# Performance work log

Hardware: AMD Instinct MI355X
Metric: run time of the kernel (lower is better)

## Reference

```python
import jax, jax.numpy as jnp
import numpy as np

B, S, D, H = 2, 2048, 1024, 16
DK = D // H


def setup_inputs() -> dict:
    key = jax.random.key(0)
    ks = jax.random.split(key, 12)
    s = 1.0 / np.sqrt(D)
    inp = {
        "key": jax.random.normal(ks[0], (B, S, D), jnp.float32),
        "query": jax.random.normal(ks[1], (B, S, D), jnp.float32),
        "value": jax.random.normal(ks[2], (B, S, D), jnp.float32),
        # causal mask, broadcastable to (B, H, S, S)
        "mask": jnp.tril(jnp.ones((S, S), jnp.int32))[None, None, :, :],
        "Wq": jax.random.normal(ks[3], (D, D), jnp.float32) * s,
        "bq": jax.random.normal(ks[4], (D,), jnp.float32) * s,
        "Wk": jax.random.normal(ks[5], (D, D), jnp.float32) * s,
        "bk": jax.random.normal(ks[6], (D,), jnp.float32) * s,
        "Wv": jax.random.normal(ks[7], (D, D), jnp.float32) * s,
        "bv": jax.random.normal(ks[8], (D,), jnp.float32) * s,
        "Wo": jax.random.normal(ks[9], (D, D), jnp.float32) * s,
        "bo": jax.random.normal(ks[10], (D,), jnp.float32) * s,
    }
    return inp


def reference(key, query, value, mask, Wq, bq, Wk, bk, Wv, bv, Wo, bo):
    # Linear projections (torch nn.Linear: x @ W.T + b)
    k = key @ Wk.T + bk
    q = query @ Wq.T + bq
    v = value @ Wv.T + bv
    # Faithful to source: raw view (B, H, S, DK), NO transpose --
    # this splits the SEQUENCE dim across heads, matching the original code.
    k = k.reshape(B, H, S, DK)
    q = q.reshape(B, H, S, DK)
    v = v.reshape(B, H, S, DK)
    # Scores scaled by sqrt(d_model) (as in source, not sqrt(d_k))
    scores = jnp.einsum('bhqd,bhkd->bhqk', q, k) / jnp.sqrt(jnp.float32(D))
    scores = jnp.where(mask == 0, -jnp.inf, scores)
    attn = jax.nn.softmax(scores, axis=-1)  # dropout p=0.0 -> identity
    x = jnp.einsum('bhqk,bhkd->bhqd', attn, v)
    # Faithful raw view merge: (B, H, S, DK) -> (B, S, H*DK)
    x = x.reshape(B, S, H * DK)
    return x @ Wo.T + bo
```

## Files before the change

kernel.cpp:

```cpp
#include <hip/hip_runtime.h>
#include <stdint.h>

typedef unsigned short u16;
typedef __attribute__((ext_vector_type(8))) short bfrag8;
typedef __attribute__((ext_vector_type(4))) float f32x4;
typedef __attribute__((ext_vector_type(8))) unsigned short u16x8;
typedef __attribute__((ext_vector_type(4))) unsigned short u16x4;

__device__ __forceinline__ u16 f2bf(float f) {
  union { float f; uint32_t u; } v; v.f = f;
  return (u16)((v.u + 0x7FFFu + ((v.u >> 16) & 1u)) >> 16);
}

__device__ __forceinline__ uint32_t cvtpk_bf16(float a, float b) {
  uint32_t r;
  asm("v_cvt_pk_bf16_f32 %0, %1, %2" : "=v"(r) : "v"(a), "v"(b));
  return r;
}

__device__ __forceinline__ void gload16(const void* g, void* l) {
  __builtin_amdgcn_global_load_lds(
      (const __attribute__((address_space(1))) void*)g,
      (__attribute__((address_space(3))) void*)l, 16, 0, 0);
}

struct CvtJob { const float* src; u16* dst; int n4; };
struct CvtBatch { CvtJob j[7]; };

__global__ void cvt_batch(CvtBatch b) {
  CvtJob jb = b.j[blockIdx.y];
  int i = blockIdx.x * blockDim.x + threadIdx.x;
  if (i >= jb.n4) return;
  float4 v = reinterpret_cast<const float4*>(jb.src)[i];
  u16x4 o;
  o[0] = f2bf(v.x); o[1] = f2bf(v.y); o[2] = f2bf(v.z); o[3] = f2bf(v.w);
  reinterpret_cast<u16x4*>(jb.dst)[i] = o;
}

struct Gemm3 {
  const u16* A[3];
  const u16* W[3];
  const float* bias[3];
  void* C[3];
};

template<int OUT_F32, int BM, int BN, int MINW>
__global__ __launch_bounds__(256, MINW) void gemm_nt_bias(Gemm3 g) {
  constexpr int K = 1024, N = 1024;
  constexpr int BK = 64;
  constexpr int WM = BM / 32, WN = BN / 32;
  __shared__ __align__(16) u16 As[2][BM][BK];
  __shared__ __align__(16) u16 Bs[2][BN][BK];
  const int z = blockIdx.z;
  const u16* __restrict__ A = g.A[z];
  const u16* __restrict__ W = g.W[z];
  const float* __restrict__ bias = g.bias[z];
  const int tid = threadIdx.x, lane = tid & 63, wave = tid >> 6;
  const int lr = lane & 15, lg = lane >> 4;
  const int wr = (wave >> 1) * (WM * 16), wc = (wave & 1) * (WN * 16);
  const int bm = blockIdx.x * BM, bn = blockIdx.y * BN;
  const int srow = lane >> 3;
  const int schunk = (lane & 7) ^ srow;

  f32x4 acc[WM][WN] = {};

  auto STAGE = [&](int k0, int bufi) {
#pragma unroll
    for (int i = 0; i < BM / 32; i++) {
      int r = wave * (BM / 4) + i * 8;
      gload16(A + (size_t)(bm + r + srow) * K + k0 + schunk * 8, &As[bufi][r][0]);
    }
#pragma unroll
    for (int i = 0; i < BN / 32; i++) {
      int r = wave * (BN / 4) + i * 8;
      gload16(W + (size_t)(bn + r + srow) * K + k0 + schunk * 8, &Bs[bufi][r][0]);
    }
  };

  STAGE(0, 0);
  __syncthreads();
  int buf = 0;

  for (int k0 = 0; k0 < K; k0 += BK) {
    if (k0 + BK < K) STAGE(k0 + BK, buf ^ 1);
    bfrag8 af[2][WM], bf[2][WN];
#pragma unroll
    for (int ks = 0; ks < 2; ks++) {
#pragma unroll
      for (int mi = 0; mi < WM; mi++) {
        const int row = wr + mi * 16 + lr;
        af[ks][mi] = *(const bfrag8*)&As[buf][row][((ks * 4 + lg) ^ (row & 7)) * 8];
      }
#pragma unroll
      for (int ni = 0; ni < WN; ni++) {
        const int row = wc + ni * 16 + lr;
        bf[ks][ni] = *(const bfrag8*)&Bs[buf][row][((ks * 4 + lg) ^ (row & 7)) * 8];
      }
    }
#pragma unroll
    for (int ks = 0; ks < 2; ks++)
#pragma unroll
      for (int mi = 0; mi < WM; mi++)
#pragma unroll
        for (int ni = 0; ni < WN; ni++)
          acc[mi][ni] = __builtin_amdgcn_mfma_f32_16x16x32_bf16(af[ks][mi], bf[ks][ni], acc[mi][ni], 0, 0, 0);
    __syncthreads();
    buf ^= 1;
  }

  const int col0 = bn + wc + lr;
#pragma unroll
  for (int ni = 0; ni < WN; ni++) {
    int col = col0 + ni * 16;
    float bv = bias[col];
#pragma unroll
    for (int mi = 0; mi < WM; mi++) {
      int row = bm + wr + mi * 16 + lg * 4;
#pragma unroll
      for (int r = 0; r < 4; r++) {
        float v = acc[mi][ni][r] + bv;
        if (OUT_F32)
          ((float*)g.C[z])[(size_t)(row + r) * N + col] = v;
        else
          ((u16*)g.C[z])[(size_t)(row + r) * N + col] = f2bf(v);
      }
    }
  }
}

__global__ void vtrans_kernel(const u16* __restrict__ Vp, u16* __restrict__ VT,
                              unsigned* __restrict__ ctr) {
  if (blockIdx.x == 0 && blockIdx.y == 0 && threadIdx.x < 8) ctr[threadIdx.x * 16] = 0u;
  __shared__ u16 T[64][66];
  const int kt = blockIdx.x, bh = blockIdx.y;
  const int tid = threadIdx.x;
  const u16* src = Vp + (size_t)bh * 131072 + (size_t)kt * 64 * 64;
#pragma unroll
  for (int i = 0; i < 2; i++) {
    int u = tid + 256 * i;
    int row = u >> 3, c = (u & 7) * 8;
    u16x8 v = *(const u16x8*)(src + row * 64 + c);
#pragma unroll
    for (int j = 0; j < 8; j++) T[c + j][row] = v[j];
  }
  __syncthreads();
  u16* dst = VT + (size_t)bh * 131072 + (size_t)kt * 64;
#pragma unroll
  for (int i = 0; i < 2; i++) {
    int u = tid + 256 * i;
    int d = u >> 3, c = (u & 7) * 8;
    u16x8 o = *(const u16x8*)&T[d][c];
    *(u16x8*)(dst + (size_t)d * 2048 + c) = o;
  }
}

__global__ __launch_bounds__(256, 3) void attn_kernel(
    const u16* __restrict__ Qp, const u16* __restrict__ Kp,
    const u16* __restrict__ VT, u16* __restrict__ X,
    unsigned* __restrict__ ctr)
{
  __shared__ __align__(16) u16 Ks[2][64][64];
  __shared__ __align__(16) u16 Vs[2][64][64];
  constexpr int LDP = 72;
  __shared__ __align__(16) u16 Ps[4][16][LDP];
  __shared__ unsigned s_unit;

  const int tid = threadIdx.x, lane = tid & 63, w = tid >> 6;
  const int lr = lane & 15, lg = lane >> 4;
  const int grp = (int)(blockIdx.x & 7);
  unsigned* __restrict__ gctr = ctr + grp * 16;
  const int srow = lane >> 3;
  const int schunk = (lane & 7) ^ srow;
  const float C2 = 0.045084939f;
  const float THR = 11.5f;

  for (;;) {
    __syncthreads();
    if (tid == 0) s_unit = atomicAdd(gctr, 1u);
    __syncthreads();
    const unsigned u = s_unit;
    if (u >= 128u) return;
    const int j = 31 - (int)(u >> 2);
    const int bh = grp * 4 + (int)(u & 3u);
    const size_t base = (size_t)bh * 131072;
    const u16* __restrict__ Qb = Qp + base;
    const u16* __restrict__ Kb = Kp + base;
    const u16* __restrict__ Vtb = VT + base;
    const int qrow0 = j * 64 + w * 16;
    const int q = qrow0 + lr;

    bfrag8 qf[2];
#pragma unroll
    for (int ds = 0; ds < 2; ds++)
      qf[ds] = *(const bfrag8*)(Qb + (size_t)(qrow0 + lr) * 64 + ds * 32 + lg * 8);

    f32x4 oacc[4] = {};
    float m_run = -INFINITY, l_run = 0.f;

    auto STAGE = [&](int kt, int bufi) {
      const u16* gk = Kb + (size_t)(kt * 64 + w * 16 + srow) * 64 + schunk * 8;
      gload16(gk,       &Ks[bufi][w * 16][0]);
      gload16(gk + 512, &Ks[bufi][w * 16 + 8][0]);
      const u16* gv = Vtb + (size_t)(w * 16 + srow) * 2048 + kt * 64 + schunk * 8;
      gload16(gv,            &Vs[bufi][w * 16][0]);
      gload16(gv + 8 * 2048, &Vs[bufi][w * 16 + 8][0]);
    };

    STAGE(0, 0);
    __syncthreads();
    int buf = 0;

    for (int kt = 0; kt <= j; kt++) {
      if (kt < j) STAGE(kt + 1, buf ^ 1);

      f32x4 sacc[4];
#pragma unroll
      for (int kf = 0; kf < 4; kf++) sacc[kf] = (f32x4){0.f, 0.f, 0.f, 0.f};
#pragma unroll
      for (int kf = 0; kf < 4; kf++) {
        const int krow = kf * 16 + lr;
        bfrag8 kb0 = *(const bfrag8*)&Ks[buf][krow][((lg) ^ (krow & 7)) * 8];
        bfrag8 kb1 = *(const bfrag8*)&Ks[buf][krow][((lg + 4) ^ (krow & 7)) * 8];
        sacc[kf] = __builtin_amdgcn_mfma_f32_16x16x32_bf16(kb0, qf[0], sacc[kf], 0, 0, 0);
        sacc[kf] = __builtin_amdgcn_mfma_f32_16x16x32_bf16(kb1, qf[1], sacc[kf], 0, 0, 0);
      }

      if (kt == j) {
#pragma unroll
        for (int kf = 0; kf < 4; kf++)
#pragma unroll
          for (int r = 0; r < 4; r++) {
            int kg = kt * 64 + kf * 16 + lg * 4 + r;
            if (kg > q) sacc[kf][r] = -INFINITY;
          }
      }

      float a0 = fmaxf(fmaxf(sacc[0][0], sacc[0][1]), fmaxf(sacc[0][2], sacc[0][3]));
      float a1 = fmaxf(fmaxf(sacc[1][0], sacc[1][1]), fmaxf(sacc[1][2], sacc[1][3]));
      float a2 = fmaxf(fmaxf(sacc[2][0], sacc[2][1]), fmaxf(sacc[2][2], sacc[2][3]));
      float a3 = fmaxf(fmaxf(sacc[3][0], sacc[3][1]), fmaxf(sacc[3][2], sacc[3][3]));
      float smax = fmaxf(fmaxf(a0, a1), fmaxf(a2, a3));
      smax = fmaxf(smax, __shfl_xor(smax, 16));
      smax = fmaxf(smax, __shfl_xor(smax, 32));
      float pmax = smax * C2;
      float mnew = m_run;
      if (!__all(pmax <= m_run + THR)) {
        mnew = fmaxf(m_run, pmax);
        float corr = __builtin_amdgcn_exp2f(m_run - mnew);
        l_run *= corr;
#pragma unroll
        for (int df = 0; df < 4; df++)
#pragma unroll
          for (int r = 0; r < 4; r++) oacc[df][r] *= corr;
        m_run = mnew;
      }

      float rs = 0.f;
#pragma unroll
      for (int kf = 0; kf < 4; kf++) {
        float p0 = __builtin_amdgcn_exp2f(__builtin_fmaf(sacc[kf][0], C2, -mnew));
        float p1 = __builtin_amdgcn_exp2f(__builtin_fmaf(sacc[kf][1], C2, -mnew));
        float p2 = __builtin_amdgcn_exp2f(__builtin_fmaf(sacc[kf][2], C2, -mnew));
        float p3 = __builtin_amdgcn_exp2f(__builtin_fmaf(sacc[kf][3], C2, -mnew));
        rs += (p0 + p1) + (p2 + p3);
        uint2 pk;
        pk.x = cvtpk_bf16(p0, p1);
        pk.y = cvtpk_bf16(p2, p3);
        *(uint2*)&Ps[w][lr][kf * 16 + lg * 4] = pk;
      }
      rs += __shfl_xor(rs, 16);
      rs += __shfl_xor(rs, 32);
      l_run += rs;

#pragma unroll
      for (int ks = 0; ks < 2; ks++) {
        bfrag8 pa = *(const bfrag8*)&Ps[w][lr][ks * 32 + lg * 8];
#pragma unroll
        for (int df = 0; df < 4; df++) {
          const int vrow = df * 16 + lr;
          bfrag8 vf = *(const bfrag8*)&Vs[buf][vrow][((ks * 4 + lg) ^ (vrow & 7)) * 8];
          oacc[df] = __builtin_amdgcn_mfma_f32_16x16x32_bf16(vf, pa, oacc[df], 0, 0, 0);
        }
      }

      __syncthreads();
      buf ^= 1;
    }

    float inv = 1.0f / l_run;
#pragma unroll
    for (int df = 0; df < 4; df++) {
      u16x4 o;
#pragma unroll
      for (int r = 0; r < 4; r++) o[r] = f2bf(oacc[df][r] * inv);
      *(u16x4*)&X[base + (size_t)q * 64 + df * 16 + lg * 4] = o;
    }
  }
}

extern "C" void kernel_launch(void* const* d_in, const int* in_sizes, int n_in,
                              void* d_out, int out_size, void* d_ws, size_t ws_size,
                              hipStream_t stream) {
  const float* key   = (const float*)d_in[0];
  const float* query = (const float*)d_in[1];
  const float* value = (const float*)d_in[2];
  const float* Wq = (const float*)d_in[4];
  const float* bq = (const float*)d_in[5];
  const float* Wk = (const float*)d_in[6];
  const float* bk = (const float*)d_in[7];
  const float* Wv = (const float*)d_in[8];
  const float* bv = (const float*)d_in[9];
  const float* Wo = (const float*)d_in[10];
  const float* bo = (const float*)d_in[11];

  u16* ws = (u16*)d_ws;
  const size_t MD = 4096ull * 1024ull;
  u16* qb  = ws;
  u16* kb  = ws + MD;
  u16* vbf = ws + 2 * MD;
  u16* Qp  = ws + 3 * MD;
  u16* Kp  = ws + 4 * MD;
  u16* Vp  = ws + 5 * MD;
  u16* Xb  = ws + 6 * MD;
  u16* wqb = ws + 7 * MD;
  u16* wkb = wqb + 1024 * 1024;
  u16* wvb = wkb + 1024 * 1024;
  u16* wob = wvb + 1024 * 1024;

  CvtBatch cb;
  cb.j[0] = { query, qb, 1048576 };
  cb.j[1] = { key,   kb, 1048576 };
  cb.j[2] = { value, vbf, 1048576 };
  cb.j[3] = { Wq, wqb, 262144 };
  cb.j[4] = { Wk, wkb, 262144 };
  cb.j[5] = { Wv, wvb, 262144 };
  cb.j[6] = { Wo, wob, 262144 };
  cvt_batch<<<dim3(4096, 7), 256, 0, stream>>>(cb);

  Gemm3 g1;
  g1.A[0] = qb;  g1.A[1] = kb;  g1.A[2] = vbf;
  g1.W[0] = wqb; g1.W[1] = wkb; g1.W[2] = wvb;
  g1.bias[0] = bq; g1.bias[1] = bk; g1.bias[2] = bv;
  g1.C[0] = Qp; g1.C[1] = Kp; g1.C[2] = Vp;
  gemm_nt_bias<0, 128, 64, 3><<<dim3(32, 16, 3), 256, 0, stream>>>(g1);

  u16* VT = vbf;
  unsigned* ctr = (unsigned*)qb;
  vtrans_kernel<<<dim3(32, 32), 256, 0, stream>>>(Vp, VT, ctr);

  attn_kernel<<<768, 256, 0, stream>>>(Qp, Kp, VT, Xb, ctr);

  Gemm3 g2;
  g2.A[0] = Xb; g2.W[0] = wob; g2.bias[0] = bo; g2.C[0] = d_out;
  g2.A[1] = g2.A[2] = nullptr; g2.W[1] = g2.W[2] = nullptr;
  g2.bias[1] = g2.bias[2] = nullptr; g2.C[1] = g2.C[2] = nullptr;
  gemm_nt_bias<1, 128, 64, 3><<<dim3(32, 16, 1), 256, 0, stream>>>(g2);
}
```

Before: 123.5 us.

## Fuse fp32-to-bf16 conversion into GEMM tile loads, drop separate convert kernel

Removes the standalone conversion kernel that turned the fp32 activations and weights into bf16 buffers. The GEMM kernel now reads fp32 tiles into registers, converts them with packed cvt instructions and writes them into swizzled LDS, prefetching one tile ahead. This saves a kernel launch and a round trip of bf16 data through global memory. In exchange the GEMM reads twice as many bytes per tile, re-converts each weight tile for every block that uses it, and holds more registers for the prefetch buffers, which may lower occupancy.

```diff
diff --git a/kernel.cpp b/kernel.cpp
--- a/kernel.cpp
+++ b/kernel.cpp
@@ -24,27 +24,14 @@
       (__attribute__((address_space(3))) void*)l, 16, 0, 0);
 }
 
-struct CvtJob { const float* src; u16* dst; int n4; };
-struct CvtBatch { CvtJob j[7]; };
-
-__global__ void cvt_batch(CvtBatch b) {
-  CvtJob jb = b.j[blockIdx.y];
-  int i = blockIdx.x * blockDim.x + threadIdx.x;
-  if (i >= jb.n4) return;
-  float4 v = reinterpret_cast<const float4*>(jb.src)[i];
-  u16x4 o;
-  o[0] = f2bf(v.x); o[1] = f2bf(v.y); o[2] = f2bf(v.z); o[3] = f2bf(v.w);
-  reinterpret_cast<u16x4*>(jb.dst)[i] = o;
-}
-
 struct Gemm3 {
-  const u16* A[3];
-  const u16* W[3];
+  const void* A[3];
+  const void* W[3];
   const float* bias[3];
   void* C[3];
 };
 
-template<int OUT_F32, int BM, int BN, int MINW>
+template<int OUT_F32, int AF32, int WF32, int BM, int BN, int MINW>
 __global__ __launch_bounds__(256, MINW) void gemm_nt_bias(Gemm3 g) {
   constexpr int K = 1024, N = 1024;
   constexpr int BK = 64;
@@ -52,8 +39,8 @@
   __shared__ __align__(16) u16 As[2][BM][BK];
   __shared__ __align__(16) u16 Bs[2][BN][BK];
   const int z = blockIdx.z;
-  const u16* __restrict__ A = g.A[z];
-  const u16* __restrict__ W = g.W[z];
+  const void* __restrict__ Ap = g.A[z];
+  const void* __restrict__ Wp = g.W[z];
   const float* __restrict__ bias = g.bias[z];
   const int tid = threadIdx.x, lane = tid & 63, wave = tid >> 6;
   const int lr = lane & 15, lg = lane >> 4;
@@ -61,28 +48,92 @@
   const int bm = blockIdx.x * BM, bn = blockIdx.y * BN;
   const int srow = lane >> 3;
   const int schunk = (lane & 7) ^ srow;
+  const int frow = lane >> 4;
+  const int fcol = (lane & 15) * 4;
+  const int fchunk = (lane & 15) >> 1;
+  const int fhalf = (lane & 1) * 4;
 
   f32x4 acc[WM][WN] = {};
-
-  auto STAGE = [&](int k0, int bufi) {
-#pragma unroll
-    for (int i = 0; i < BM / 32; i++) {
-      int r = wave * (BM / 4) + i * 8;
-      gload16(A + (size_t)(bm + r + srow) * K + k0 + schunk * 8, &As[bufi][r][0]);
-    }
-#pragma unroll
-    for (int i = 0; i < BN / 32; i++) {
-      int r = wave * (BN / 4) + i * 8;
-      gload16(W + (size_t)(bn + r + srow) * K + k0 + schunk * 8, &Bs[bufi][r][0]);
-    }
-  };
-
-  STAGE(0, 0);
+  float4 ra[AF32 ? BM / 16 : 1];
+  float4 rw[WF32 ? BN / 16 : 1];
+
+  auto LOAD_A = [&](int k0) {
+    if constexpr (AF32) {
+      const float* Af = (const float*)Ap;
+#pragma unroll
+      for (int i = 0; i < BM / 16; i++) {
+        int row = wave * (BM / 4) + i * 4 + frow;
+        ra[i] = *(const float4*)(Af + (size_t)(bm + row) * K + k0 + fcol);
+      }
+    }
+  };
+  auto WRITE_A = [&](int bufi) {
+    if constexpr (AF32) {
+#pragma unroll
+      for (int i = 0; i < BM / 16; i++) {
+        int row = wave * (BM / 4) + i * 4 + frow;
+        uint2 p;
+        p.x = cvtpk_bf16(ra[i].x, ra[i].y);
+        p.y = cvtpk_bf16(ra[i].z, ra[i].w);
+        *(uint2*)&As[bufi][row][(fchunk ^ (row & 7)) * 8 + fhalf] = p;
+      }
+    }
+  };
+  auto GLOAD_A = [&](int k0, int bufi) {
+    if constexpr (!AF32) {
+      const u16* Ab = (const u16*)Ap;
+#pragma unroll
+      for (int i = 0; i < BM / 32; i++) {
+        int r = wave * (BM / 4) + i * 8;
+        gload16(Ab + (size_t)(bm + r + srow) * K + k0 + schunk * 8, &As[bufi][r][0]);
+      }
+    }
+  };
+  auto LOAD_W = [&](int k0) {
+    if constexpr (WF32) {
+      const float* Wf = (const float*)Wp;
+#pragma unroll
+      for (int i = 0; i < BN / 16; i++) {
+        int row = wave * (BN / 4) + i * 4 + frow;
+        rw[i] = *(const float4*)(Wf + (size_t)(bn + row) * K + k0 + fcol);
+      }
+    }
+  };
+  auto WRITE_W = [&](int bufi) {
+    if constexpr (WF32) {
+#pragma unroll
+      for (int i = 0; i < BN / 16; i++) {
+        int row = wave * (BN / 4) + i * 4 + frow;
+        uint2 p;
+        p.x = cvtpk_bf16(rw[i].x, rw[i].y);
+        p.y = cvtpk_bf16(rw[i].z, rw[i].w);
+        *(uint2*)&Bs[bufi][row][(fchunk ^ (row & 7)) * 8 + fhalf] = p;
+      }
+    }
+  };
+  auto GLOAD_W = [&](int k0, int bufi) {
+    if constexpr (!WF32) {
+      const u16* Wb = (const u16*)Wp;
+#pragma unroll
+      for (int i = 0; i < BN / 32; i++) {
+        int r = wave * (BN / 4) + i * 8;
+        gload16(Wb + (size_t)(bn + r + srow) * K + k0 + schunk * 8, &Bs[bufi][r][0]);
+      }
+    }
+  };
+
+  LOAD_A(0); LOAD_W(0);
+  WRITE_A(0); WRITE_W(0);
+  GLOAD_A(0, 0); GLOAD_W(0, 0);
   __syncthreads();
   int buf = 0;
 
   for (int k0 = 0; k0 < K; k0 += BK) {
-    if (k0 + BK < K) STAGE(k0 + BK, buf ^ 1);
+    const bool pf = (k0 + BK < K);
+    if (pf) {
+      GLOAD_A(k0 + BK, buf ^ 1); GLOAD_W(k0 + BK, buf ^ 1);
+      LOAD_A(k0 + BK); LOAD_W(k0 + BK);
+    }
     bfrag8 af[2][WM], bf[2][WN];
 #pragma unroll
     for (int ks = 0; ks < 2; ks++) {
@@ -104,6 +155,7 @@
 #pragma unroll
         for (int ni = 0; ni < WN; ni++)
           acc[mi][ni] = __builtin_amdgcn_mfma_f32_16x16x32_bf16(af[ks][mi], bf[ks][ni], acc[mi][ni], 0, 0, 0);
+    if (pf) { WRITE_A(buf ^ 1); WRITE_W(buf ^ 1); }
     __syncthreads();
     buf ^= 1;
   }
@@ -315,44 +367,29 @@
 
   u16* ws = (u16*)d_ws;
   const size_t MD = 4096ull * 1024ull;
-  u16* qb  = ws;
-  u16* kb  = ws + MD;
-  u16* vbf = ws + 2 * MD;
+  u16* scratch = ws;
+  u16* vtbuf = ws + 2 * MD;
   u16* Qp  = ws + 3 * MD;
   u16* Kp  = ws + 4 * MD;
   u16* Vp  = ws + 5 * MD;
   u16* Xb  = ws + 6 * MD;
-  u16* wqb = ws + 7 * MD;
-  u16* wkb = wqb + 1024 * 1024;
-  u16* wvb = wkb + 1024 * 1024;
-  u16* wob = wvb + 1024 * 1024;
-
-  CvtBatch cb;
-  cb.j[0] = { query, qb, 1048576 };
-  cb.j[1] = { key,   kb, 1048576 };
-  cb.j[2] = { value, vbf, 1048576 };
-  cb.j[3] = { Wq, wqb, 262144 };
-  cb.j[4] = { Wk, wkb, 262144 };
-  cb.j[5] = { Wv, wvb, 262144 };
-  cb.j[6] = { Wo, wob, 262144 };
-  cvt_batch<<<dim3(4096, 7), 256, 0, stream>>>(cb);
 
   Gemm3 g1;
-  g1.A[0] = qb;  g1.A[1] = kb;  g1.A[2] = vbf;
-  g1.W[0] = wqb; g1.W[1] = wkb; g1.W[2] = wvb;
+  g1.A[0] = query; g1.A[1] = key; g1.A[2] = value;
+  g1.W[0] = Wq;    g1.W[1] = Wk;  g1.W[2] = Wv;
   g1.bias[0] = bq; g1.bias[1] = bk; g1.bias[2] = bv;
   g1.C[0] = Qp; g1.C[1] = Kp; g1.C[2] = Vp;
-  gemm_nt_bias<0, 128, 64, 3><<<dim3(32, 16, 3), 256, 0, stream>>>(g1);
-
-  u16* VT = vbf;
-  unsigned* ctr = (unsigned*)qb;
+  gemm_nt_bias<0, 1, 1, 128, 64, 3><<<dim3(32, 16, 3), 256, 0, stream>>>(g1);
+
+  u16* VT = vtbuf;
+  unsigned* ctr = (unsigned*)scratch;
   vtrans_kernel<<<dim3(32, 32), 256, 0, stream>>>(Vp, VT, ctr);
 
   attn_kernel<<<768, 256, 0, stream>>>(Qp, Kp, VT, Xb, ctr);
 
   Gemm3 g2;
-  g2.A[0] = Xb; g2.W[0] = wob; g2.bias[0] = bo; g2.C[0] = d_out;
+  g2.A[0] = Xb; g2.W[0] = Wo; g2.bias[0] = bo; g2.C[0] = d_out;
   g2.A[1] = g2.A[2] = nullptr; g2.W[1] = g2.W[2] = nullptr;
   g2.bias[1] = g2.bias[2] = nullptr; g2.C[1] = g2.C[2] = nullptr;
-  gemm_nt_bias<1, 128, 64, 3><<<dim3(32, 16, 1), 256, 0, stream>>>(g2);
-}
+  gemm_nt_bias<1, 0, 1, 128, 64, 3><<<dim3(32, 16, 1), 256, 0, stream>>>(g2);
+}
```

Result: slower. 128.2 us (+3.8%).

## Double attention key tile to 128 and interleave softmax with PV per half

Applied to the files above, without the earlier changes.

The attention inner loop now processes 128 keys per iteration instead of 64. K and V^T staging is widened to match, with a 16-chunk XOR swizzle for V. The exp/pack of P and the PV MFMAs are split into two 64-key halves so the small per-wave P buffer can be reused. This halves the number of block barriers and online-softmax rescale checks per query tile. In exchange it uses more LDS and registers: occupancy drops from 3 to 2 blocks per CU, the grid shrinks to 512, and the masked diagonal tile can waste up to 64 extra keys of compute.

```diff
diff --git a/kernel.cpp b/kernel.cpp
--- a/kernel.cpp
+++ b/kernel.cpp
@@ -154,13 +154,13 @@
   }
 }
 
-__global__ __launch_bounds__(256, 3) void attn_kernel(
+__global__ __launch_bounds__(256, 2) void attn_kernel(
     const u16* __restrict__ Qp, const u16* __restrict__ Kp,
     const u16* __restrict__ VT, u16* __restrict__ X,
     unsigned* __restrict__ ctr)
 {
-  __shared__ __align__(16) u16 Ks[2][64][64];
-  __shared__ __align__(16) u16 Vs[2][64][64];
+  __shared__ __align__(16) u16 Ks[2][128][64];
+  __shared__ __align__(16) u16 Vs[2][64][128];
   constexpr int LDP = 72;
   __shared__ __align__(16) u16 Ps[4][16][LDP];
   __shared__ unsigned s_unit;
@@ -169,8 +169,10 @@
   const int lr = lane & 15, lg = lane >> 4;
   const int grp = (int)(blockIdx.x & 7);
   unsigned* __restrict__ gctr = ctr + grp * 16;
-  const int srow = lane >> 3;
-  const int schunk = (lane & 7) ^ srow;
+  const int srow8 = lane >> 3;
+  const int schunk8 = (lane & 7) ^ srow8;
+  const int srow4 = lane >> 4;
+  const int lane16 = lane & 15;
   const float C2 = 0.045084939f;
   const float THR = 11.5f;
 
@@ -198,26 +200,34 @@
     float m_run = -INFINITY, l_run = 0.f;
 
     auto STAGE = [&](int kt, int bufi) {
-      const u16* gk = Kb + (size_t)(kt * 64 + w * 16 + srow) * 64 + schunk * 8;
-      gload16(gk,       &Ks[bufi][w * 16][0]);
-      gload16(gk + 512, &Ks[bufi][w * 16 + 8][0]);
-      const u16* gv = Vtb + (size_t)(w * 16 + srow) * 2048 + kt * 64 + schunk * 8;
-      gload16(gv,            &Vs[bufi][w * 16][0]);
-      gload16(gv + 8 * 2048, &Vs[bufi][w * 16 + 8][0]);
+#pragma unroll
+      for (int i = 0; i < 4; i++) {
+        int r = w * 32 + i * 8;
+        gload16(Kb + (size_t)(kt * 128 + r + srow8) * 64 + schunk8 * 8, &Ks[bufi][r][0]);
+      }
+#pragma unroll
+      for (int i = 0; i < 4; i++) {
+        int r = w * 16 + i * 4;
+        int row = r + srow4;
+        gload16(Vtb + (size_t)row * 2048 + kt * 128 + (lane16 ^ (row & 15)) * 8,
+                &Vs[bufi][r][0]);
+      }
     };
+
+    const int ktmax = (j * 64 + 63) >> 7;
 
     STAGE(0, 0);
     __syncthreads();
     int buf = 0;
 
-    for (int kt = 0; kt <= j; kt++) {
-      if (kt < j) STAGE(kt + 1, buf ^ 1);
-
-      f32x4 sacc[4];
-#pragma unroll
-      for (int kf = 0; kf < 4; kf++) sacc[kf] = (f32x4){0.f, 0.f, 0.f, 0.f};
-#pragma unroll
-      for (int kf = 0; kf < 4; kf++) {
+    for (int kt = 0; kt <= ktmax; kt++) {
+      if (kt < ktmax) STAGE(kt + 1, buf ^ 1);
+
+      f32x4 sacc[8];
+#pragma unroll
+      for (int kf = 0; kf < 8; kf++) sacc[kf] = (f32x4){0.f, 0.f, 0.f, 0.f};
+#pragma unroll
+      for (int kf = 0; kf < 8; kf++) {
         const int krow = kf * 16 + lr;
         bfrag8 kb0 = *(const bfrag8*)&Ks[buf][krow][((lg) ^ (krow & 7)) * 8];
         bfrag8 kb1 = *(const bfrag8*)&Ks[buf][krow][((lg + 4) ^ (krow & 7)) * 8];
@@ -225,21 +235,26 @@
         sacc[kf] = __builtin_amdgcn_mfma_f32_16x16x32_bf16(kb1, qf[1], sacc[kf], 0, 0, 0);
       }
 
-      if (kt == j) {
-#pragma unroll
-        for (int kf = 0; kf < 4; kf++)
+      if (kt == ktmax) {
+#pragma unroll
+        for (int kf = 0; kf < 8; kf++)
 #pragma unroll
           for (int r = 0; r < 4; r++) {
-            int kg = kt * 64 + kf * 16 + lg * 4 + r;
+            int kg = kt * 128 + kf * 16 + lg * 4 + r;
             if (kg > q) sacc[kf][r] = -INFINITY;
           }
       }
 
-      float a0 = fmaxf(fmaxf(sacc[0][0], sacc[0][1]), fmaxf(sacc[0][2], sacc[0][3]));
-      float a1 = fmaxf(fmaxf(sacc[1][0], sacc[1][1]), fmaxf(sacc[1][2], sacc[1][3]));
-      float a2 = fmaxf(fmaxf(sacc[2][0], sacc[2][1]), fmaxf(sacc[2][2], sacc[2][3]));
-      float a3 = fmaxf(fmaxf(sacc[3][0], sacc[3][1]), fmaxf(sacc[3][2], sacc[3][3]));
-      float smax = fmaxf(fmaxf(a0, a1), fmaxf(a2, a3));
+      float b0 = fmaxf(fmaxf(sacc[0][0], sacc[0][1]), fmaxf(sacc[0][2], sacc[0][3]));
+      float b1 = fmaxf(fmaxf(sacc[1][0], sacc[1][1]), fmaxf(sacc[1][2], sacc[1][3]));
+      float b2 = fmaxf(fmaxf(sacc[2][0], sacc[2][1]), fmaxf(sacc[2][2], sacc[2][3]));
+      float b3 = fmaxf(fmaxf(sacc[3][0], sacc[3][1]), fmaxf(sacc[3][2], sacc[3][3]));
+      float b4 = fmaxf(fmaxf(sacc[4][0], sacc[4][1]), fmaxf(sacc[4][2], sacc[4][3]));
+      float b5 = fmaxf(fmaxf(sacc[5][0], sacc[5][1]), fmaxf(sacc[5][2], sacc[5][3]));
+      float b6 = fmaxf(fmaxf(sacc[6][0], sacc[6][1]), fmaxf(sacc[6][2], sacc[6][3]));
+      float b7 = fmaxf(fmaxf(sacc[7][0], sacc[7][1]), fmaxf(sacc[7][2], sacc[7][3]));
+      float smax = fmaxf(fmaxf(fmaxf(b0, b1), fmaxf(b2, b3)),
+                         fmaxf(fmaxf(b4, b5), fmaxf(b6, b7)));
       smax = fmaxf(smax, __shfl_xor(smax, 16));
       smax = fmaxf(smax, __shfl_xor(smax, 32));
       float pmax = smax * C2;
@@ -257,31 +272,34 @@
 
       float rs = 0.f;
 #pragma unroll
-      for (int kf = 0; kf < 4; kf++) {
-        float p0 = __builtin_amdgcn_exp2f(__builtin_fmaf(sacc[kf][0], C2, -mnew));
-        float p1 = __builtin_amdgcn_exp2f(__builtin_fmaf(sacc[kf][1], C2, -mnew));
-        float p2 = __builtin_amdgcn_exp2f(__builtin_fmaf(sacc[kf][2], C2, -mnew));
-        float p3 = __builtin_amdgcn_exp2f(__builtin_fmaf(sacc[kf][3], C2, -mnew));
-        rs += (p0 + p1) + (p2 + p3);
-        uint2 pk;
-        pk.x = cvtpk_bf16(p0, p1);
-        pk.y = cvtpk_bf16(p2, p3);
-        *(uint2*)&Ps[w][lr][kf * 16 + lg * 4] = pk;
+      for (int h = 0; h < 2; h++) {
+#pragma unroll
+        for (int kf2 = 0; kf2 < 4; kf2++) {
+          const int kf = h * 4 + kf2;
+          float p0 = __builtin_amdgcn_exp2f(__builtin_fmaf(sacc[kf][0], C2, -mnew));
+          float p1 = __builtin_amdgcn_exp2f(__builtin_fmaf(sacc[kf][1], C2, -mnew));
+          float p2 = __builtin_amdgcn_exp2f(__builtin_fmaf(sacc[kf][2], C2, -mnew));
+          float p3 = __builtin_amdgcn_exp2f(__builtin_fmaf(sacc[kf][3], C2, -mnew));
+          rs += (p0 + p1) + (p2 + p3);
+          uint2 pk;
+          pk.x = cvtpk_bf16(p0, p1);
+          pk.y = cvtpk_bf16(p2, p3);
+          *(uint2*)&Ps[w][lr][kf2 * 16 + lg * 4] = pk;
+        }
+#pragma unroll
+        for (int ks = 0; ks < 2; ks++) {
+          bfrag8 pa = *(const bfrag8*)&Ps[w][lr][ks * 32 + lg * 8];
+#pragma unroll
+          for (int df = 0; df < 4; df++) {
+            const int vrow = df * 16 + lr;
+            bfrag8 vf = *(const bfrag8*)&Vs[buf][vrow][((h * 8 + ks * 4 + lg) ^ (vrow & 15)) * 8];
+            oacc[df] = __builtin_amdgcn_mfma_f32_16x16x32_bf16(vf, pa, oacc[df], 0, 0, 0);
+          }
+        }
       }
       rs += __shfl_xor(rs, 16);
       rs += __shfl_xor(rs, 32);
       l_run += rs;
-
-#pragma unroll
-      for (int ks = 0; ks < 2; ks++) {
-        bfrag8 pa = *(const bfrag8*)&Ps[w][lr][ks * 32 + lg * 8];
-#pragma unroll
-        for (int df = 0; df < 4; df++) {
-          const int vrow = df * 16 + lr;
-          bfrag8 vf = *(const bfrag8*)&Vs[buf][vrow][((ks * 4 + lg) ^ (vrow & 7)) * 8];
-          oacc[df] = __builtin_amdgcn_mfma_f32_16x16x32_bf16(vf, pa, oacc[df], 0, 0, 0);
-        }
-      }
 
       __syncthreads();
       buf ^= 1;
@@ -348,7 +366,7 @@
   unsigned* ctr = (unsigned*)qb;
   vtrans_kernel<<<dim3(32, 32), 256, 0, stream>>>(Vp, VT, ctr);
 
-  attn_kernel<<<768, 256, 0, stream>>>(Qp, Kp, VT, Xb, ctr);
+  attn_kernel<<<512, 256, 0, stream>>>(Qp, Kp, VT, Xb, ctr);
 
   Gemm3 g2;
   g2.A[0] = Xb; g2.W[0] = wob; g2.bias[0] = bo; g2.C[0] = d_out;
```

Result: no change. 123.2 us (-0.2%).
